# Kernel tuning notes

Hardware: AMD Instinct MI355X
Metric: run time of the kernel (lower is better)

The kernel has to match this reference:

```python
import jax, jax.numpy as jnp
import numpy as np

NUM_EMBEDDINGS = 1024
EMBEDDING_DIM = 64


def setup_inputs() -> dict:
    key = jax.random.key(0)
    kx, kw = jax.random.split(key)
    x = jax.random.normal(kx, (16, 4096, EMBEDDING_DIM), dtype=jnp.float32)
    # torch init: uniform(-1/K, 1/K)
    bound = 1.0 / NUM_EMBEDDINGS
    weight = jax.random.uniform(kw, (NUM_EMBEDDINGS, EMBEDDING_DIM),
                                dtype=jnp.float32, minval=-bound, maxval=bound)
    return {"x": x, "weight": weight}


def reference(x, weight):
    flat_x = x.reshape(-1, EMBEDDING_DIM)                      # [N, D]
    x_sq = jnp.sum(flat_x ** 2, axis=1, keepdims=True)
    w_sq = jnp.sum(weight ** 2, axis=1)[None, :]
    distances = x_sq - 2.0 * (flat_x @ weight.T) + w_sq
    encoding_indices = jnp.argmin(distances, axis=1)           # [N]
    quantized = weight[encoding_indices]                       # [N, D]
    e_latent_loss = jnp.mean((jax.lax.stop_gradient(quantized) - flat_x) ** 2)
    q_latent_loss = jnp.mean((quantized - jax.lax.stop_gradient(flat_x)) ** 2)
    loss = q_latent_loss + 0.25 * e_latent_loss
    # straight-through estimator
    quantized = flat_x + jax.lax.stop_gradient(quantized - flat_x)
    return quantized.reshape(x.shape), encoding_indices, loss
```

## Files before the change

### kernel.cpp

```cpp
#include <hip/hip_runtime.h>
#include <math.h>

#define EMB_D 64
#define MARGIN 6.0e-5f

typedef float  f32x4  __attribute__((ext_vector_type(4)));
typedef short  bf16x8 __attribute__((ext_vector_type(8)));

__device__ __forceinline__ unsigned short f2bf(float f) {
    unsigned int u = __float_as_uint(f);
    return (unsigned short)((u + 0x7FFFu + ((u >> 16) & 1u)) >> 16);
}
__device__ __forceinline__ float bf2f(unsigned short h) {
    return __uint_as_float(((unsigned int)h) << 16);
}

union Pack8 { ushort u[8]; bf16x8 v; uint4 q; };

__device__ __forceinline__ bf16x8 ldbf8(const unsigned short* p) {
    union { uint4 u; bf16x8 v; } c;
    c.u = *(const uint4*)p;
    return c.v;
}

__global__ __launch_bounds__(256)
void vq_prepw_kernel(const float* __restrict__ w,
                     unsigned short* __restrict__ wt_hi,
                     unsigned short* __restrict__ wt_lo,
                     float* __restrict__ wsq, float* __restrict__ loss_out,
                     int K) {
    const int i = blockIdx.x * 256 + threadIdx.x;
    if (i == 0) loss_out[0] = 0.f;
    if (i >= K * 8) return;
    const int krow = i >> 3, q = i & 7;
    const int dest = ((krow >> 6) << 9) + (((krow >> 4) & 3) << 7) + (q << 4)
                   + (krow & 15);
    const float* src = w + (size_t)krow * EMB_D + q * 8;
    Pack8 h, l;
#pragma unroll
    for (int j = 0; j < 8; ++j) {
        const float f = src[j];
        h.u[j] = f2bf(f);
        l.u[j] = f2bf(f - bf2f(h.u[j]));
    }
    ((uint4*)wt_hi)[dest] = h.q;
    ((uint4*)wt_lo)[dest] = l.q;

    if (i < K) {
        const float* wr = w + (size_t)i * EMB_D;
        float r[8];
#pragma unroll
        for (int j = 0; j < 8; ++j) r[j] = __fmul_rn(wr[j], wr[j]);
#pragma unroll
        for (int t = 1; t < 8; ++t)
#pragma unroll
            for (int j = 0; j < 8; ++j)
                r[j] = __fadd_rn(r[j], __fmul_rn(wr[t * 8 + j], wr[t * 8 + j]));
        float a = __fadd_rn(__fadd_rn(r[0], r[1]), __fadd_rn(r[2], r[3]));
        float b = __fadd_rn(__fadd_rn(r[4], r[5]), __fadd_rn(r[6], r[7]));
        wsq[i] = __fadd_rn(a, b);
    }
}

__global__ __launch_bounds__(256, 4)
void vq_screen_kernel(const float* __restrict__ x,
                      const unsigned short* __restrict__ wt_hi,
                      const unsigned short* __restrict__ wt_lo,
                      const float* __restrict__ wsq, int* __restrict__ fidx,
                      int* __restrict__ status, int* __restrict__ k2arr,
                      int K, int N) {
    const int tid  = threadIdx.x;
    const int lane = tid & 63;
    const int wave = tid >> 6;
    const int quad = lane >> 4;
    const int c16  = lane & 15;
    const int rowbase = blockIdx.x * 64 + wave * 16;

    __shared__ uint4 sh4[512];
    __shared__ uint4 sl4[512];
    __shared__ float wsq_lds[1024];
    __shared__ float M1[4][16][17], M2[4][16][17];
    __shared__ int   N1[4][16][17], N2[4][16][17];

    const float* xrow = x + (size_t)(rowbase + c16) * EMB_D + quad * 8;
    Pack8 ah0, al0, ah1, al1;
#pragma unroll
    for (int j = 0; j < 8; ++j) {
        const float f0 = xrow[j];
        ah0.u[j] = f2bf(f0); al0.u[j] = f2bf(f0 - bf2f(ah0.u[j]));
        const float f1 = xrow[32 + j];
        ah1.u[j] = f2bf(f1); al1.u[j] = f2bf(f1 - bf2f(ah1.u[j]));
    }
    const bf16x8 ahi0 = ah0.v, alo0 = al0.v, ahi1 = ah1.v, alo1 = al1.v;

    ((float4*)wsq_lds)[tid] = ((const float4*)wsq)[tid];

    float s1[4], s2[4];
    int   k1[4], k2[4];
#pragma unroll
    for (int i = 0; i < 4; ++i) {
        s1[i] = INFINITY; s2[i] = INFINITY; k1[i] = 0; k2[i] = 0;
    }

    const uint4* gh = (const uint4*)wt_hi;
    const uint4* gl = (const uint4*)wt_lo;
    uint4 ph0 = gh[tid], ph1 = gh[256 + tid];
    uint4 pl0 = gl[tid], pl1 = gl[256 + tid];

    const int nseg = K >> 6;
    for (int seg = 0; seg < nseg; ++seg) {
        sh4[tid] = ph0; sh4[256 + tid] = ph1;
        sl4[tid] = pl0; sl4[256 + tid] = pl1;
        __syncthreads();
        if (seg + 1 < nseg) {
            const int b = (seg + 1) * 512;
            ph0 = gh[b + tid]; ph1 = gh[b + 256 + tid];
            pl0 = gl[b + tid]; pl1 = gl[b + 256 + tid];
        }

#pragma unroll
        for (int s = 0; s < 4; ++s) {
            const unsigned short* shp = (const unsigned short*)sh4;
            const unsigned short* slp = (const unsigned short*)sl4;
            const bf16x8 bhi0 = ldbf8(shp + (s * 128 + lane) * 8);
            const bf16x8 bhi1 = ldbf8(shp + (s * 128 + 64 + lane) * 8);
            const bf16x8 blo0 = ldbf8(slp + (s * 128 + lane) * 8);
            const bf16x8 blo1 = ldbf8(slp + (s * 128 + 64 + lane) * 8);

            f32x4 acc0 = {0.f, 0.f, 0.f, 0.f};
            f32x4 acc1 = {0.f, 0.f, 0.f, 0.f};
            acc0 = __builtin_amdgcn_mfma_f32_16x16x32_bf16(alo0, bhi0, acc0, 0, 0, 0);
            acc1 = __builtin_amdgcn_mfma_f32_16x16x32_bf16(alo1, bhi1, acc1, 0, 0, 0);
            acc0 = __builtin_amdgcn_mfma_f32_16x16x32_bf16(ahi0, blo0, acc0, 0, 0, 0);
            acc1 = __builtin_amdgcn_mfma_f32_16x16x32_bf16(ahi1, blo1, acc1, 0, 0, 0);
            acc0 = __builtin_amdgcn_mfma_f32_16x16x32_bf16(ahi0, bhi0, acc0, 0, 0, 0);
            acc1 = __builtin_amdgcn_mfma_f32_16x16x32_bf16(ahi1, bhi1, acc1, 0, 0, 0);

            const int   kk = seg * 64 + s * 16 + c16;
            const float wq = wsq_lds[kk];
#pragma unroll
            for (int i = 0; i < 4; ++i) {
                const float sc = fmaf(-2.0f, acc0[i] + acc1[i], wq);
                const bool c1 = sc < s1[i];
                const bool c2 = sc < s2[i];
                k2[i] = c1 ? k1[i] : (c2 ? kk : k2[i]);
                k1[i] = c1 ? kk : k1[i];
                s2[i] = __builtin_amdgcn_fmed3f(sc, s1[i], s2[i]);
                s1[i] = fminf(sc, s1[i]);
            }
        }
        __syncthreads();
    }

#pragma unroll
    for (int i = 0; i < 4; ++i) {
        const int r16 = quad * 4 + i;
        M1[wave][r16][c16] = s1[i];  N1[wave][r16][c16] = k1[i];
        M2[wave][r16][c16] = s2[i];  N2[wave][r16][c16] = k2[i];
    }
    __syncthreads();
    if (lane < 16) {
        float g1 = INFINITY, g2 = INFINITY, g3 = INFINITY;
        int   gk1 = 0, gk2 = 0;
#pragma unroll
        for (int c = 0; c < 16; ++c) {
#pragma unroll
            for (int h = 0; h < 2; ++h) {
                const float s = h == 0 ? M1[wave][lane][c] : M2[wave][lane][c];
                const int   k = h == 0 ? N1[wave][lane][c] : N2[wave][lane][c];
                if (s < g1)      { g3 = g2; g2 = g1; gk2 = gk1; g1 = s; gk1 = k; }
                else if (s < g2) { g3 = g2; g2 = s; gk2 = k; }
                else if (s < g3) { g3 = s; }
            }
        }
        const int row = rowbase + lane;
        fidx[row] = gk1;
        int st = 0;
        if (g2 - g1 <= MARGIN) st = (g3 - g1 > MARGIN) ? 1 : 2;
        status[row] = st;
        if (st == 1) k2arr[row] = gk2;
    }
}

__global__ __launch_bounds__(256)
void vq_gather_kernel(const float* __restrict__ x, const float* __restrict__ w,
                      const float* __restrict__ wsq, const int* __restrict__ fidx,
                      const int* __restrict__ status, const int* __restrict__ k2arr,
                      float* __restrict__ out, float* __restrict__ loss_out,
                      int N, int K, float scale) {
    const int tid  = threadIdx.x;
    const int lane = tid & 63;
    const int wave = tid >> 6;
    __shared__ int kf[64];
    __shared__ int strow[64];
    if (tid < 64) {
        const int row = blockIdx.x * 64 + tid;
        kf[tid]    = fidx[row];
        strow[tid] = status[row];
    }
    __syncthreads();

    if (tid < 64 && strow[tid] == 1) {
        const int row = blockIdx.x * 64 + tid;
        const int ka = kf[tid], kb = k2arr[row];
        const float4* xp = (const float4*)(x + (size_t)row * EMB_D);
        const float4* wa = (const float4*)(w + (size_t)ka * EMB_D);
        const float4* wb = (const float4*)(w + (size_t)kb * EMB_D);
        float r[8];
        double aa0 = 0, aa1 = 0, aa2 = 0, aa3 = 0;
        double ab0 = 0, ab1 = 0, ab2 = 0, ab3 = 0;
#pragma unroll
        for (int q = 0; q < 16; ++q) {
            const float4 xv = xp[q], va = wa[q], vb = wb[q];
            const int j = (q & 1) * 4;
            if (q < 2) {
                r[j + 0] = __fmul_rn(xv.x, xv.x);
                r[j + 1] = __fmul_rn(xv.y, xv.y);
                r[j + 2] = __fmul_rn(xv.z, xv.z);
                r[j + 3] = __fmul_rn(xv.w, xv.w);
            } else {
                r[j + 0] = __fadd_rn(r[j + 0], __fmul_rn(xv.x, xv.x));
                r[j + 1] = __fadd_rn(r[j + 1], __fmul_rn(xv.y, xv.y));
                r[j + 2] = __fadd_rn(r[j + 2], __fmul_rn(xv.z, xv.z));
                r[j + 3] = __fadd_rn(r[j + 3], __fmul_rn(xv.w, xv.w));
            }
            aa0 = fma((double)xv.x, (double)va.x, aa0);
            aa1 = fma((double)xv.y, (double)va.y, aa1);
            aa2 = fma((double)xv.z, (double)va.z, aa2);
            aa3 = fma((double)xv.w, (double)va.w, aa3);
            ab0 = fma((double)xv.x, (double)vb.x, ab0);
            ab1 = fma((double)xv.y, (double)vb.y, ab1);
            ab2 = fma((double)xv.z, (double)vb.z, ab2);
            ab3 = fma((double)xv.w, (double)vb.w, ab3);
        }
        const float xsq = __fadd_rn(
            __fadd_rn(__fadd_rn(r[0], r[1]), __fadd_rn(r[2], r[3])),
            __fadd_rn(__fadd_rn(r[4], r[5]), __fadd_rn(r[6], r[7])));
        const float mfa = (float)((aa0 + aa1) + (aa2 + aa3));
        const float mfb = (float)((ab0 + ab1) + (ab2 + ab3));
        const float sa = __fadd_rn(__fsub_rn(xsq, __fmul_rn(2.0f, mfa)), wsq[ka]);
        const float sb = __fadd_rn(__fsub_rn(xsq, __fmul_rn(2.0f, mfb)), wsq[kb]);
        int win = ka;
        if (sb < sa || (sb == sa && kb < ka)) win = kb;
        kf[tid] = win;
    }
    __syncthreads();

    __shared__ float4 xs4[16];
    __shared__ float  xsqs;
    __shared__ float  ls[256];
    __shared__ int    lk[256];
    for (int i = 0; i < 64; ++i) {
        if (strow[i] != 2) continue;
        const int row = blockIdx.x * 64 + i;
        if (tid < 16) xs4[tid] = ((const float4*)(x + (size_t)row * EMB_D))[tid];
        __syncthreads();
        if (tid == 0) {
            const float* xf = (const float*)xs4;
            float r[8];
#pragma unroll
            for (int j = 0; j < 8; ++j) r[j] = __fmul_rn(xf[j], xf[j]);
#pragma unroll
            for (int t = 1; t < 8; ++t)
#pragma unroll
                for (int j = 0; j < 8; ++j)
                    r[j] = __fadd_rn(r[j], __fmul_rn(xf[t * 8 + j], xf[t * 8 + j]));
            xsqs = __fadd_rn(
                __fadd_rn(__fadd_rn(r[0], r[1]), __fadd_rn(r[2], r[3])),
                __fadd_rn(__fadd_rn(r[4], r[5]), __fadd_rn(r[6], r[7])));
        }
        __syncthreads();
        const float xsq = xsqs;

        float bs = INFINITY;
        int   bk = K;
        for (int t = 0; t < 4; ++t) {
            const int k = wave * (K >> 2) + t * 64 + lane;
            const float4* wr4 = (const float4*)(w + (size_t)k * EMB_D);
            double a0 = 0.0, a1 = 0.0, a2 = 0.0, a3 = 0.0;
#pragma unroll
            for (int q = 0; q < EMB_D / 4; ++q) {
                const float4 xv = xs4[q];
                const float4 wv = wr4[q];
                a0 = fma((double)xv.x, (double)wv.x, a0);
                a1 = fma((double)xv.y, (double)wv.y, a1);
                a2 = fma((double)xv.z, (double)wv.z, a2);
                a3 = fma((double)xv.w, (double)wv.w, a3);
            }
            const float mf = (float)((a0 + a1) + (a2 + a3));
            const float t2 = __fsub_rn(xsq, __fmul_rn(2.0f, mf));
            const float sc = __fadd_rn(t2, wsq[k]);
            if (sc < bs || (sc == bs && k < bk)) { bs = sc; bk = k; }
        }
        ls[tid] = bs; lk[tid] = bk;
        __syncthreads();
        if (wave == 0) {
            float gs = ls[lane];
            int   gk = lk[lane];
#pragma unroll
            for (int c = 1; c < 4; ++c) {
                const float os = ls[c * 64 + lane];
                const int   ok = lk[c * 64 + lane];
                if (os < gs || (os == gs && ok < gk)) { gs = os; gk = ok; }
            }
#pragma unroll
            for (int off = 32; off > 0; off >>= 1) {
                const float os = __shfl_down(gs, off);
                const int   ok = __shfl_down(gk, off);
                if (os < gs || (os == gs && ok < gk)) { gs = os; gk = ok; }
            }
            if (lane == 0) kf[i] = gk;
        }
        __syncthreads();
    }

    if (tid < 64) {
        const int row = blockIdx.x * 64 + tid;
        out[(size_t)N * EMB_D + row] = (float)kf[tid];
    }
    float lpart = 0.f;
#pragma unroll
    for (int rep = 0; rep < 4; ++rep) {
        int f4   = rep * 256 + tid;
        int rr   = f4 >> 4;
        int c    = f4 & 15;
        int k    = kf[rr];
        int grow = blockIdx.x * 64 + rr;
        float4 wv = ((const float4*)(w + (size_t)k * EMB_D))[c];
        float4 xq = ((const float4*)(x + (size_t)grow * EMB_D))[c];
        ((float4*)out)[(size_t)grow * (EMB_D / 4) + c] = wv;
        float dx = wv.x - xq.x, dy = wv.y - xq.y;
        float dz = wv.z - xq.z, dw = wv.w - xq.w;
        lpart += dx * dx + dy * dy + dz * dz + dw * dw;
    }
#pragma unroll
    for (int off = 32; off > 0; off >>= 1) lpart += __shfl_down(lpart, off);
    __shared__ float lred[4];
    if (lane == 0) lred[wave] = lpart;
    __syncthreads();
    if (tid == 0)
        atomicAdd(loss_out, ((lred[0] + lred[1]) + (lred[2] + lred[3])) * scale);
}

extern "C" void kernel_launch(void* const* d_in, const int* in_sizes, int n_in,
                              void* d_out, int out_size, void* d_ws, size_t ws_size,
                              hipStream_t stream) {
    const float* x = (const float*)d_in[0];
    const float* w = (const float*)d_in[1];
    float* out = (float*)d_out;
    const int xsz = in_sizes[0];
    const int wsz = in_sizes[1];
    const int N   = xsz / EMB_D;
    const int K   = wsz / EMB_D;
    const int NB  = N / 64;
    float* loss_out = out + (size_t)N * EMB_D + N;

    int*   status = (int*)d_ws;
    int*   k2arr  = status + N;
    int*   fidx   = k2arr + N;
    float* wsq    = (float*)(fidx + N);
    unsigned short* wt_hi = (unsigned short*)(wsq + K);
    unsigned short* wt_lo = wt_hi + (size_t)K * EMB_D;

    vq_prepw_kernel<<<(K * 8 + 255) / 256, 256, 0, stream>>>(w, wt_hi, wt_lo,
                                                             wsq, loss_out, K);
    vq_screen_kernel<<<NB, 256, 0, stream>>>(x, wt_hi, wt_lo, wsq, fidx,
                                             status, k2arr, K, N);
    vq_gather_kernel<<<NB, 256, 0, stream>>>(x, w, wsq, fidx, status, k2arr,
                                             out, loss_out, N, K,
                                             1.25f / (float)xsz);
}
```

Measured before the change: 150.4 us.

## Fuse screen and gather kernels, double rows per wave, pack index into score bits

Merges the screening and gather kernels into one, so the per-row index/status arrays stay in shared memory and are never written to or read back from global memory. Each wave now handles 32 rows (two 16-row MFMA tiles), so each LDS codebook tile is reused across twice as many rows. The running top-2 tracking packs a 6-bit segment index into the low mantissa bits of a biased (kept positive) score and uses unsigned min/max in place of separate index selects. Risks: lower occupancy (launch bounds 2), half as many blocks, and a score truncated by 6 mantissa bits, which could affect tie and margin decisions.

Result: faster. 135.3 us (-10.0%).

```diff
diff --git a/kernel.cpp b/kernel.cpp
--- a/kernel.cpp
+++ b/kernel.cpp
@@ -3,6 +3,7 @@
 
 #define EMB_D 64
 #define MARGIN 6.0e-5f
+#define SBIAS 0.5f
 
 typedef float  f32x4  __attribute__((ext_vector_type(4)));
 typedef short  bf16x8 __attribute__((ext_vector_type(8)));
@@ -62,45 +63,55 @@
     }
 }
 
-__global__ __launch_bounds__(256, 4)
-void vq_screen_kernel(const float* __restrict__ x,
-                      const unsigned short* __restrict__ wt_hi,
-                      const unsigned short* __restrict__ wt_lo,
-                      const float* __restrict__ wsq, int* __restrict__ fidx,
-                      int* __restrict__ status, int* __restrict__ k2arr,
-                      int K, int N) {
+__global__ __launch_bounds__(256, 2)
+void vq_fused_kernel(const float* __restrict__ x,
+                     const unsigned short* __restrict__ wt_hi,
+                     const unsigned short* __restrict__ wt_lo,
+                     const float* __restrict__ wsq,
+                     const float* __restrict__ w,
+                     float* __restrict__ out, float* __restrict__ loss_out,
+                     int K, int N, float scale) {
     const int tid  = threadIdx.x;
     const int lane = tid & 63;
     const int wave = tid >> 6;
     const int quad = lane >> 4;
     const int c16  = lane & 15;
-    const int rowbase = blockIdx.x * 64 + wave * 16;
+    const int rowbase = blockIdx.x * 128 + wave * 32;
 
     __shared__ uint4 sh4[512];
     __shared__ uint4 sl4[512];
     __shared__ float wsq_lds[1024];
-    __shared__ float M1[4][16][17], M2[4][16][17];
-    __shared__ int   N1[4][16][17], N2[4][16][17];
-
-    const float* xrow = x + (size_t)(rowbase + c16) * EMB_D + quad * 8;
-    Pack8 ah0, al0, ah1, al1;
-#pragma unroll
-    for (int j = 0; j < 8; ++j) {
-        const float f0 = xrow[j];
-        ah0.u[j] = f2bf(f0); al0.u[j] = f2bf(f0 - bf2f(ah0.u[j]));
-        const float f1 = xrow[32 + j];
-        ah1.u[j] = f2bf(f1); al1.u[j] = f2bf(f1 - bf2f(ah1.u[j]));
-    }
-    const bf16x8 ahi0 = ah0.v, alo0 = al0.v, ahi1 = ah1.v, alo1 = al1.v;
-
-    ((float4*)wsq_lds)[tid] = ((const float4*)wsq)[tid];
-
-    float s1[4], s2[4];
-    int   k1[4], k2[4];
-#pragma unroll
-    for (int i = 0; i < 4; ++i) {
-        s1[i] = INFINITY; s2[i] = INFINITY; k1[i] = 0; k2[i] = 0;
-    }
+    __shared__ float M1[4][32][17], M2[4][32][17];
+    __shared__ int   N1[4][32][17], N2[4][32][17];
+    __shared__ int   kf[128], strow[128], k2row[128];
+
+    Pack8 AH0[2], AL0[2], AH1[2], AL1[2];
+#pragma unroll
+    for (int t = 0; t < 2; ++t) {
+        const float* xrow =
+            x + (size_t)(rowbase + t * 16 + c16) * EMB_D + quad * 8;
+#pragma unroll
+        for (int j = 0; j < 8; ++j) {
+            const float f0 = xrow[j];
+            AH0[t].u[j] = f2bf(f0);
+            AL0[t].u[j] = f2bf(f0 - bf2f(AH0[t].u[j]));
+            const float f1 = xrow[32 + j];
+            AH1[t].u[j] = f2bf(f1);
+            AL1[t].u[j] = f2bf(f1 - bf2f(AH1[t].u[j]));
+        }
+    }
+
+    {
+        float4 wv = ((const float4*)wsq)[tid];
+        wv.x += SBIAS; wv.y += SBIAS; wv.z += SBIAS; wv.w += SBIAS;
+        ((float4*)wsq_lds)[tid] = wv;
+    }
+
+    unsigned s1v[2][4], s2v[2][4];
+#pragma unroll
+    for (int t = 0; t < 2; ++t)
+#pragma unroll
+        for (int i = 0; i < 4; ++i) { s1v[t][i] = 0xFFFFFFFFu; s2v[t][i] = 0xFFFFFFFFu; }
 
     const uint4* gh = (const uint4*)wt_hi;
     const uint4* gl = (const uint4*)wt_lo;
@@ -126,83 +137,73 @@
             const bf16x8 bhi1 = ldbf8(shp + (s * 128 + 64 + lane) * 8);
             const bf16x8 blo0 = ldbf8(slp + (s * 128 + lane) * 8);
             const bf16x8 blo1 = ldbf8(slp + (s * 128 + 64 + lane) * 8);
-
-            f32x4 acc0 = {0.f, 0.f, 0.f, 0.f};
-            f32x4 acc1 = {0.f, 0.f, 0.f, 0.f};
-            acc0 = __builtin_amdgcn_mfma_f32_16x16x32_bf16(alo0, bhi0, acc0, 0, 0, 0);
-            acc1 = __builtin_amdgcn_mfma_f32_16x16x32_bf16(alo1, bhi1, acc1, 0, 0, 0);
-            acc0 = __builtin_amdgcn_mfma_f32_16x16x32_bf16(ahi0, blo0, acc0, 0, 0, 0);
-            acc1 = __builtin_amdgcn_mfma_f32_16x16x32_bf16(ahi1, blo1, acc1, 0, 0, 0);
-            acc0 = __builtin_amdgcn_mfma_f32_16x16x32_bf16(ahi0, bhi0, acc0, 0, 0, 0);
-            acc1 = __builtin_amdgcn_mfma_f32_16x16x32_bf16(ahi1, bhi1, acc1, 0, 0, 0);
-
-            const int   kk = seg * 64 + s * 16 + c16;
-            const float wq = wsq_lds[kk];
-#pragma unroll
-            for (int i = 0; i < 4; ++i) {
-                const float sc = fmaf(-2.0f, acc0[i] + acc1[i], wq);
-                const bool c1 = sc < s1[i];
-                const bool c2 = sc < s2[i];
-                k2[i] = c1 ? k1[i] : (c2 ? kk : k2[i]);
-                k1[i] = c1 ? kk : k1[i];
-                s2[i] = __builtin_amdgcn_fmed3f(sc, s1[i], s2[i]);
-                s1[i] = fminf(sc, s1[i]);
-            }
-        }
-        __syncthreads();
-    }
-
-#pragma unroll
-    for (int i = 0; i < 4; ++i) {
-        const int r16 = quad * 4 + i;
-        M1[wave][r16][c16] = s1[i];  N1[wave][r16][c16] = k1[i];
-        M2[wave][r16][c16] = s2[i];  N2[wave][r16][c16] = k2[i];
-    }
+            const float wqb = wsq_lds[seg * 64 + s * 16 + c16];
+            const unsigned idx6 = (unsigned)(seg * 4 + s);
+
+#pragma unroll
+            for (int t = 0; t < 2; ++t) {
+                f32x4 acc = {0.f, 0.f, 0.f, 0.f};
+                acc = __builtin_amdgcn_mfma_f32_16x16x32_bf16(AL0[t].v, bhi0, acc, 0, 0, 0);
+                acc = __builtin_amdgcn_mfma_f32_16x16x32_bf16(AH0[t].v, blo0, acc, 0, 0, 0);
+                acc = __builtin_amdgcn_mfma_f32_16x16x32_bf16(AL1[t].v, bhi1, acc, 0, 0, 0);
+                acc = __builtin_amdgcn_mfma_f32_16x16x32_bf16(AH1[t].v, blo1, acc, 0, 0, 0);
+                acc = __builtin_amdgcn_mfma_f32_16x16x32_bf16(AH0[t].v, bhi0, acc, 0, 0, 0);
+                acc = __builtin_amdgcn_mfma_f32_16x16x32_bf16(AH1[t].v, bhi1, acc, 0, 0, 0);
+#pragma unroll
+                for (int i = 0; i < 4; ++i) {
+                    const float sc = fmaf(-2.0f, acc[i], wqb);
+                    const unsigned p =
+                        (__float_as_uint(sc) & 0xFFFFFFC0u) | idx6;
+                    const unsigned m = p > s1v[t][i] ? p : s1v[t][i];
+                    s2v[t][i] = s2v[t][i] < m ? s2v[t][i] : m;
+                    s1v[t][i] = s1v[t][i] < p ? s1v[t][i] : p;
+                }
+            }
+        }
+        __syncthreads();
+    }
+
+#pragma unroll
+    for (int t = 0; t < 2; ++t)
+#pragma unroll
+        for (int i = 0; i < 4; ++i) {
+            const int r32 = t * 16 + quad * 4 + i;
+            M1[wave][r32][c16] = __uint_as_float(s1v[t][i] & 0xFFFFFFC0u);
+            N1[wave][r32][c16] = (int)(((s1v[t][i] & 63u) << 4) | (unsigned)c16);
+            M2[wave][r32][c16] = __uint_as_float(s2v[t][i] & 0xFFFFFFC0u);
+            N2[wave][r32][c16] = (int)(((s2v[t][i] & 63u) << 4) | (unsigned)c16);
+        }
     __syncthreads();
     if (lane < 16) {
-        float g1 = INFINITY, g2 = INFINITY, g3 = INFINITY;
-        int   gk1 = 0, gk2 = 0;
-#pragma unroll
-        for (int c = 0; c < 16; ++c) {
-#pragma unroll
-            for (int h = 0; h < 2; ++h) {
-                const float s = h == 0 ? M1[wave][lane][c] : M2[wave][lane][c];
-                const int   k = h == 0 ? N1[wave][lane][c] : N2[wave][lane][c];
-                if (s < g1)      { g3 = g2; g2 = g1; gk2 = gk1; g1 = s; gk1 = k; }
-                else if (s < g2) { g3 = g2; g2 = s; gk2 = k; }
-                else if (s < g3) { g3 = s; }
-            }
-        }
-        const int row = rowbase + lane;
-        fidx[row] = gk1;
-        int st = 0;
-        if (g2 - g1 <= MARGIN) st = (g3 - g1 > MARGIN) ? 1 : 2;
-        status[row] = st;
-        if (st == 1) k2arr[row] = gk2;
-    }
-}
-
-__global__ __launch_bounds__(256)
-void vq_gather_kernel(const float* __restrict__ x, const float* __restrict__ w,
-                      const float* __restrict__ wsq, const int* __restrict__ fidx,
-                      const int* __restrict__ status, const int* __restrict__ k2arr,
-                      float* __restrict__ out, float* __restrict__ loss_out,
-                      int N, int K, float scale) {
-    const int tid  = threadIdx.x;
-    const int lane = tid & 63;
-    const int wave = tid >> 6;
-    __shared__ int kf[64];
-    __shared__ int strow[64];
-    if (tid < 64) {
-        const int row = blockIdx.x * 64 + tid;
-        kf[tid]    = fidx[row];
-        strow[tid] = status[row];
+#pragma unroll
+        for (int rep = 0; rep < 2; ++rep) {
+            const int r = rep * 16 + lane;
+            float g1 = INFINITY, g2 = INFINITY, g3 = INFINITY;
+            int   gk1 = 0, gk2 = 0;
+#pragma unroll
+            for (int c = 0; c < 16; ++c) {
+#pragma unroll
+                for (int h = 0; h < 2; ++h) {
+                    const float s = h == 0 ? M1[wave][r][c] : M2[wave][r][c];
+                    const int   k = h == 0 ? N1[wave][r][c] : N2[wave][r][c];
+                    if (s < g1)      { g3 = g2; g2 = g1; gk2 = gk1; g1 = s; gk1 = k; }
+                    else if (s < g2) { g3 = g2; g2 = s; gk2 = k; }
+                    else if (s < g3) { g3 = s; }
+                }
+            }
+            const int lr = wave * 32 + r;
+            kf[lr] = gk1;
+            int st = 0;
+            if (g2 - g1 <= MARGIN) st = (g3 - g1 > MARGIN) ? 1 : 2;
+            strow[lr] = st;
+            k2row[lr] = gk2;
+        }
     }
     __syncthreads();
 
-    if (tid < 64 && strow[tid] == 1) {
-        const int row = blockIdx.x * 64 + tid;
-        const int ka = kf[tid], kb = k2arr[row];
+    if (tid < 128 && strow[tid] == 1) {
+        const int row = blockIdx.x * 128 + tid;
+        const int ka = kf[tid], kb = k2row[tid];
         const float4* xp = (const float4*)(x + (size_t)row * EMB_D);
         const float4* wa = (const float4*)(w + (size_t)ka * EMB_D);
         const float4* wb = (const float4*)(w + (size_t)kb * EMB_D);
@@ -250,9 +251,9 @@
     __shared__ float  xsqs;
     __shared__ float  ls[256];
     __shared__ int    lk[256];
-    for (int i = 0; i < 64; ++i) {
+    for (int i = 0; i < 128; ++i) {
         if (strow[i] != 2) continue;
-        const int row = blockIdx.x * 64 + i;
+        const int row = blockIdx.x * 128 + i;
         if (tid < 16) xs4[tid] = ((const float4*)(x + (size_t)row * EMB_D))[tid];
         __syncthreads();
         if (tid == 0) {
@@ -314,18 +315,18 @@
         __syncthreads();
     }
 
-    if (tid < 64) {
-        const int row = blockIdx.x * 64 + tid;
+    if (tid < 128) {
+        const int row = blockIdx.x * 128 + tid;
         out[(size_t)N * EMB_D + row] = (float)kf[tid];
     }
     float lpart = 0.f;
 #pragma unroll
-    for (int rep = 0; rep < 4; ++rep) {
+    for (int rep = 0; rep < 8; ++rep) {
         int f4   = rep * 256 + tid;
         int rr   = f4 >> 4;
         int c    = f4 & 15;
         int k    = kf[rr];
-        int grow = blockIdx.x * 64 + rr;
+        int grow = blockIdx.x * 128 + rr;
         float4 wv = ((const float4*)(w + (size_t)k * EMB_D))[c];
         float4 xq = ((const float4*)(x + (size_t)grow * EMB_D))[c];
         ((float4*)out)[(size_t)grow * (EMB_D / 4) + c] = wv;
@@ -352,21 +353,16 @@
     const int wsz = in_sizes[1];
     const int N   = xsz / EMB_D;
     const int K   = wsz / EMB_D;
-    const int NB  = N / 64;
+    const int NB  = N / 128;
     float* loss_out = out + (size_t)N * EMB_D + N;
 
-    int*   status = (int*)d_ws;
-    int*   k2arr  = status + N;
-    int*   fidx   = k2arr + N;
-    float* wsq    = (float*)(fidx + N);
+    float* wsq = (float*)d_ws;
     unsigned short* wt_hi = (unsigned short*)(wsq + K);
     unsigned short* wt_lo = wt_hi + (size_t)K * EMB_D;
 
     vq_prepw_kernel<<<(K * 8 + 255) / 256, 256, 0, stream>>>(w, wt_hi, wt_lo,
                                                              wsq, loss_out, K);
-    vq_screen_kernel<<<NB, 256, 0, stream>>>(x, wt_hi, wt_lo, wsq, fidx,
-                                             status, k2arr, K, N);
-    vq_gather_kernel<<<NB, 256, 0, stream>>>(x, w, wsq, fidx, status, k2arr,
-                                             out, loss_out, N, K,
-                                             1.25f / (float)xsz);
-}
+    vq_fused_kernel<<<NB, 256, 0, stream>>>(x, wt_hi, wt_lo, wsq, w, out,
+                                            loss_out, K, N,
+                                            1.25f / (float)xsz);
+}
```
